# Kernel tuning notes

Hardware: AMD Instinct MI355X
Metric: run time of the kernel (lower is better)

Reference implementation:

```python
import jax, jax.numpy as jnp
import numpy as np

LN_EPS = 1e-5      # torch nn.LayerNorm default
NORM_EPS = 1e-12   # torch F.normalize default


def _layer_norm(x, gamma, beta):
    mu = jnp.mean(x, axis=-1, keepdims=True)
    var = jnp.mean(jnp.square(x - mu), axis=-1, keepdims=True)
    return (x - mu) * jax.lax.rsqrt(var + LN_EPS) * gamma + beta


def setup_inputs() -> dict:
    key = jax.random.key(0)
    ks = jax.random.split(key, 5)
    B, H, W = 4, 480, 712
    N = B * H * W
    x = jax.random.normal(ks[0], (N, 64), dtype=jnp.float32)
    # torch Linear default init ~ U(-1/sqrt(fan_in), 1/sqrt(fan_in)); scaled normals are fine here
    w1 = jax.random.normal(ks[1], (64, 32), dtype=jnp.float32) * (1.0 / np.sqrt(64))
    w2 = jax.random.normal(ks[2], (32, 16), dtype=jnp.float32) * (1.0 / np.sqrt(32))
    w3 = jax.random.normal(ks[3], (16, 3), dtype=jnp.float32) * (1.0 / np.sqrt(16))
    b3 = jax.random.normal(ks[4], (3,), dtype=jnp.float32) * 0.01
    return {
        "x": x,
        "w1": w1, "g1": jnp.ones((32,), jnp.float32), "b1": jnp.zeros((32,), jnp.float32),
        "w2": w2, "g2": jnp.ones((16,), jnp.float32), "b2": jnp.zeros((16,), jnp.float32),
        "w3": w3, "b3": b3,
        "B": B, "H": H, "W": W,
    }


def reference(x, w1, g1, b1, w2, g2, b2, w3, b3, B, H, W):
    # decoder: Linear(64,32,no bias) -> LN(32) -> ReLU -> Linear(32,16,no bias) -> LN(16) -> ReLU -> Linear(16,3)
    h = jax.nn.relu(_layer_norm(x @ w1, g1, b1))
    h = jax.nn.relu(_layer_norm(h @ w2, g2, b2))
    out2d = h @ w3 + b3                      # [B*H*W, 3]
    # reshape_for_layer_norm(..., reverse=True): [B*H*W, C] -> [B, C, H, W]
    out = out2d.reshape(B, H, W, 3).transpose(0, 3, 1, 2)
    # F.normalize(out, dim=1): x / max(||x||_2, eps) along channel dim
    n = jnp.sqrt(jnp.sum(jnp.square(out), axis=1, keepdims=True))
    return out / jnp.maximum(n, NORM_EPS)
```

## Files before the change

### kernel.cpp

```cpp
#include <hip/hip_runtime.h>
#include <stdint.h>

#define LN_EPS 1e-5f

__global__ __launch_bounds__(256, 4) void dec_kernel(
    const float* __restrict__ x,
    const float* __restrict__ w1, const float* __restrict__ g1, const float* __restrict__ b1,
    const float* __restrict__ w2, const float* __restrict__ g2, const float* __restrict__ b2,
    const float* __restrict__ w3, const float* __restrict__ b3,
    float* __restrict__ out, int N, int HW)
{
  const int row = blockIdx.x * 256 + threadIdx.x;
  if (row >= N) return;

  const float4* __restrict__ xp = (const float4*)(x + (size_t)row * 64);

  float4 xv[16];
#pragma unroll
  for (int c = 0; c < 16; ++c) xv[c] = xp[c];

  float acc[32];
#pragma unroll
  for (int j = 0; j < 32; ++j) acc[j] = 0.f;

#pragma unroll
  for (int c = 0; c < 16; ++c) {
#pragma unroll
    for (int kk = 0; kk < 4; ++kk) {
      float xk = (kk == 0) ? xv[c].x : (kk == 1) ? xv[c].y : (kk == 2) ? xv[c].z : xv[c].w;
      const float* wrow = w1 + (c * 4 + kk) * 32;
#pragma unroll
      for (int j = 0; j < 32; ++j) acc[j] = fmaf(xk, wrow[j], acc[j]);
    }
  }

  {
    float p0 = 0.f, p1 = 0.f, p2 = 0.f, p3 = 0.f;
#pragma unroll
    for (int j = 0; j < 32; j += 4) { p0 += acc[j]; p1 += acc[j+1]; p2 += acc[j+2]; p3 += acc[j+3]; }
    float mu = ((p0 + p1) + (p2 + p3)) * 0.03125f;
    float q0 = 0.f, q1 = 0.f, q2 = 0.f, q3 = 0.f;
#pragma unroll
    for (int j = 0; j < 32; j += 4) {
      float d0 = acc[j] - mu, d1 = acc[j+1] - mu, d2 = acc[j+2] - mu, d3 = acc[j+3] - mu;
      acc[j] = d0; acc[j+1] = d1; acc[j+2] = d2; acc[j+3] = d3;
      q0 = fmaf(d0, d0, q0); q1 = fmaf(d1, d1, q1); q2 = fmaf(d2, d2, q2); q3 = fmaf(d3, d3, q3);
    }
    float var = ((q0 + q1) + (q2 + q3)) * 0.03125f;
    float rs  = rsqrtf(var + LN_EPS);
#pragma unroll
    for (int j = 0; j < 32; ++j) {
      float t = acc[j] * rs;
      t = fmaf(t, g1[j], b1[j]);
      acc[j] = fmaxf(t, 0.f);
    }
  }

  float a2[16];
#pragma unroll
  for (int j = 0; j < 16; ++j) a2[j] = 0.f;
#pragma unroll
  for (int k = 0; k < 32; ++k) {
    float hk = acc[k];
    const float* wrow = w2 + k * 16;
#pragma unroll
    for (int j = 0; j < 16; ++j) a2[j] = fmaf(hk, wrow[j], a2[j]);
  }
  {
    float p0 = 0.f, p1 = 0.f, p2 = 0.f, p3 = 0.f;
#pragma unroll
    for (int j = 0; j < 16; j += 4) { p0 += a2[j]; p1 += a2[j+1]; p2 += a2[j+2]; p3 += a2[j+3]; }
    float mu = ((p0 + p1) + (p2 + p3)) * 0.0625f;
    float q0 = 0.f, q1 = 0.f, q2 = 0.f, q3 = 0.f;
#pragma unroll
    for (int j = 0; j < 16; j += 4) {
      float d0 = a2[j] - mu, d1 = a2[j+1] - mu, d2 = a2[j+2] - mu, d3 = a2[j+3] - mu;
      a2[j] = d0; a2[j+1] = d1; a2[j+2] = d2; a2[j+3] = d3;
      q0 = fmaf(d0, d0, q0); q1 = fmaf(d1, d1, q1); q2 = fmaf(d2, d2, q2); q3 = fmaf(d3, d3, q3);
    }
    float var = ((q0 + q1) + (q2 + q3)) * 0.0625f;
    float rs  = rsqrtf(var + LN_EPS);
#pragma unroll
    for (int j = 0; j < 16; ++j) {
      float t = a2[j] * rs;
      t = fmaf(t, g2[j], b2[j]);
      a2[j] = fmaxf(t, 0.f);
    }
  }

  float o0 = b3[0], o1 = b3[1], o2 = b3[2];
#pragma unroll
  for (int k = 0; k < 16; ++k) {
    float hk = a2[k];
    o0 = fmaf(hk, w3[k * 3 + 0], o0);
    o1 = fmaf(hk, w3[k * 3 + 1], o1);
    o2 = fmaf(hk, w3[k * 3 + 2], o2);
  }
  float nsq = fmaf(o0, o0, fmaf(o1, o1, o2 * o2));
  float inv = rsqrtf(fmaxf(nsq, 1e-24f));
  o0 *= inv; o1 *= inv; o2 *= inv;

  int b = (int)((unsigned)row / (unsigned)HW);
  int p = row - b * HW;
  size_t obase = (size_t)b * 3 * HW + p;
  out[obase]          = o0;
  out[obase + HW]     = o1;
  out[obase + 2 * HW] = o2;
}

extern "C" void kernel_launch(void* const* d_in, const int* in_sizes, int n_in,
                              void* d_out, int out_size, void* d_ws, size_t ws_size,
                              hipStream_t stream) {
  const float* x  = (const float*)d_in[0];
  const float* w1 = (const float*)d_in[1];
  const float* g1 = (const float*)d_in[2];
  const float* b1 = (const float*)d_in[3];
  const float* w2 = (const float*)d_in[4];
  const float* g2 = (const float*)d_in[5];
  const float* b2 = (const float*)d_in[6];
  const float* w3 = (const float*)d_in[7];
  const float* b3 = (const float*)d_in[8];
  float* out = (float*)d_out;

  const int N  = in_sizes[0] / 64;
  const int HW = N / 4;
  const int nblocks = (N + 255) / 256;
  dec_kernel<<<nblocks, 256, 0, stream>>>(x, w1, g1, b1, w2, g2, b2, w3, b3, out, N, HW);
}
```

Before: 575.3 us.

## Use persistent grid-stride loop with software-pipelined half-row input prefetch

Launches a fixed grid of up to 1024 blocks that loop over rows in grid-stride order. Each row's 64 floats are loaded in two halves, and the first half of the next row is prefetched while the second half of the current row is being multiplied. sched_barrier calls stop the compiler from reordering loads across these points. The aim is to hide global-load latency with register double-buffering; the cost is higher register pressure, with launch bounds relaxed to 3 blocks per SM and fewer waves in flight.

```diff
diff --git a/kernel.cpp b/kernel.cpp
--- a/kernel.cpp
+++ b/kernel.cpp
@@ -3,109 +3,140 @@
 
 #define LN_EPS 1e-5f
 
-__global__ __launch_bounds__(256, 4) void dec_kernel(
+__global__ __launch_bounds__(256, 3) void dec_kernel(
     const float* __restrict__ x,
     const float* __restrict__ w1, const float* __restrict__ g1, const float* __restrict__ b1,
     const float* __restrict__ w2, const float* __restrict__ g2, const float* __restrict__ b2,
     const float* __restrict__ w3, const float* __restrict__ b3,
     float* __restrict__ out, int N, int HW)
 {
-  const int row = blockIdx.x * 256 + threadIdx.x;
+  const int stride = gridDim.x * 256;
+  int row = blockIdx.x * 256 + threadIdx.x;
   if (row >= N) return;
 
-  const float4* __restrict__ xp = (const float4*)(x + (size_t)row * 64);
+  float4 bufA[8], bufB[8];
+  {
+    const float4* __restrict__ xp = (const float4*)(x + (size_t)row * 64);
+#pragma unroll
+    for (int c = 0; c < 8; ++c) bufA[c] = xp[c];
+  }
 
-  float4 xv[16];
+  while (true) {
+    const float4* __restrict__ xc = (const float4*)(x + (size_t)row * 64);
 #pragma unroll
-  for (int c = 0; c < 16; ++c) xv[c] = xp[c];
+    for (int c = 0; c < 8; ++c) bufB[c] = xc[c + 8];
+    __builtin_amdgcn_sched_barrier(0);
 
-  float acc[32];
+    float acc[32];
 #pragma unroll
-  for (int j = 0; j < 32; ++j) acc[j] = 0.f;
+    for (int j = 0; j < 32; ++j) acc[j] = 0.f;
+#pragma unroll
+    for (int c = 0; c < 8; ++c) {
+#pragma unroll
+      for (int kk = 0; kk < 4; ++kk) {
+        float xk = (kk == 0) ? bufA[c].x : (kk == 1) ? bufA[c].y : (kk == 2) ? bufA[c].z : bufA[c].w;
+        const float* wrow = w1 + (c * 4 + kk) * 32;
+#pragma unroll
+        for (int j = 0; j < 32; ++j) acc[j] = fmaf(xk, wrow[j], acc[j]);
+      }
+    }
+
+    const int nrow = row + stride;
+    {
+      const int prow = (nrow < N) ? nrow : row;
+      const float4* __restrict__ xn = (const float4*)(x + (size_t)prow * 64);
+#pragma unroll
+      for (int c = 0; c < 8; ++c) bufA[c] = xn[c];
+    }
+    __builtin_amdgcn_sched_barrier(0);
 
 #pragma unroll
-  for (int c = 0; c < 16; ++c) {
+    for (int c = 0; c < 8; ++c) {
 #pragma unroll
-    for (int kk = 0; kk < 4; ++kk) {
-      float xk = (kk == 0) ? xv[c].x : (kk == 1) ? xv[c].y : (kk == 2) ? xv[c].z : xv[c].w;
-      const float* wrow = w1 + (c * 4 + kk) * 32;
+      for (int kk = 0; kk < 4; ++kk) {
+        float xk = (kk == 0) ? bufB[c].x : (kk == 1) ? bufB[c].y : (kk == 2) ? bufB[c].z : bufB[c].w;
+        const float* wrow = w1 + (32 + c * 4 + kk) * 32;
 #pragma unroll
-      for (int j = 0; j < 32; ++j) acc[j] = fmaf(xk, wrow[j], acc[j]);
+        for (int j = 0; j < 32; ++j) acc[j] = fmaf(xk, wrow[j], acc[j]);
+      }
     }
+
+    {
+      float p0 = 0.f, p1 = 0.f, p2 = 0.f, p3 = 0.f;
+#pragma unroll
+      for (int j = 0; j < 32; j += 4) { p0 += acc[j]; p1 += acc[j+1]; p2 += acc[j+2]; p3 += acc[j+3]; }
+      float mu = ((p0 + p1) + (p2 + p3)) * 0.03125f;
+      float q0 = 0.f, q1 = 0.f, q2 = 0.f, q3 = 0.f;
+#pragma unroll
+      for (int j = 0; j < 32; j += 4) {
+        float d0 = acc[j] - mu, d1 = acc[j+1] - mu, d2 = acc[j+2] - mu, d3 = acc[j+3] - mu;
+        acc[j] = d0; acc[j+1] = d1; acc[j+2] = d2; acc[j+3] = d3;
+        q0 = fmaf(d0, d0, q0); q1 = fmaf(d1, d1, q1); q2 = fmaf(d2, d2, q2); q3 = fmaf(d3, d3, q3);
+      }
+      float var = ((q0 + q1) + (q2 + q3)) * 0.03125f;
+      float rs  = rsqrtf(var + LN_EPS);
+#pragma unroll
+      for (int j = 0; j < 32; ++j) {
+        float t = acc[j] * rs;
+        t = fmaf(t, g1[j], b1[j]);
+        acc[j] = fmaxf(t, 0.f);
+      }
+    }
+
+    float a2[16];
+#pragma unroll
+    for (int j = 0; j < 16; ++j) a2[j] = 0.f;
+#pragma unroll
+    for (int k = 0; k < 32; ++k) {
+      float hk = acc[k];
+      const float* wrow = w2 + k * 16;
+#pragma unroll
+      for (int j = 0; j < 16; ++j) a2[j] = fmaf(hk, wrow[j], a2[j]);
+    }
+    {
+      float p0 = 0.f, p1 = 0.f, p2 = 0.f, p3 = 0.f;
+#pragma unroll
+      for (int j = 0; j < 16; j += 4) { p0 += a2[j]; p1 += a2[j+1]; p2 += a2[j+2]; p3 += a2[j+3]; }
+      float mu = ((p0 + p1) + (p2 + p3)) * 0.0625f;
+      float q0 = 0.f, q1 = 0.f, q2 = 0.f, q3 = 0.f;
+#pragma unroll
+      for (int j = 0; j < 16; j += 4) {
+        float d0 = a2[j] - mu, d1 = a2[j+1] - mu, d2 = a2[j+2] - mu, d3 = a2[j+3] - mu;
+        a2[j] = d0; a2[j+1] = d1; a2[j+2] = d2; a2[j+3] = d3;
+        q0 = fmaf(d0, d0, q0); q1 = fmaf(d1, d1, q1); q2 = fmaf(d2, d2, q2); q3 = fmaf(d3, d3, q3);
+      }
+      float var = ((q0 + q1) + (q2 + q3)) * 0.0625f;
+      float rs  = rsqrtf(var + LN_EPS);
+#pragma unroll
+      for (int j = 0; j < 16; ++j) {
+        float t = a2[j] * rs;
+        t = fmaf(t, g2[j], b2[j]);
+        a2[j] = fmaxf(t, 0.f);
+      }
+    }
+
+    float o0 = b3[0], o1 = b3[1], o2 = b3[2];
+#pragma unroll
+    for (int k = 0; k < 16; ++k) {
+      float hk = a2[k];
+      o0 = fmaf(hk, w3[k * 3 + 0], o0);
+      o1 = fmaf(hk, w3[k * 3 + 1], o1);
+      o2 = fmaf(hk, w3[k * 3 + 2], o2);
+    }
+    float nsq = fmaf(o0, o0, fmaf(o1, o1, o2 * o2));
+    float inv = rsqrtf(fmaxf(nsq, 1e-24f));
+    o0 *= inv; o1 *= inv; o2 *= inv;
+
+    int b = (int)((unsigned)row / (unsigned)HW);
+    int p = row - b * HW;
+    size_t obase = (size_t)b * 3 * HW + p;
+    out[obase]          = o0;
+    out[obase + HW]     = o1;
+    out[obase + 2 * HW] = o2;
+
+    if (nrow >= N) break;
+    row = nrow;
   }
-
-  {
-    float p0 = 0.f, p1 = 0.f, p2 = 0.f, p3 = 0.f;
-#pragma unroll
-    for (int j = 0; j < 32; j += 4) { p0 += acc[j]; p1 += acc[j+1]; p2 += acc[j+2]; p3 += acc[j+3]; }
-    float mu = ((p0 + p1) + (p2 + p3)) * 0.03125f;
-    float q0 = 0.f, q1 = 0.f, q2 = 0.f, q3 = 0.f;
-#pragma unroll
-    for (int j = 0; j < 32; j += 4) {
-      float d0 = acc[j] - mu, d1 = acc[j+1] - mu, d2 = acc[j+2] - mu, d3 = acc[j+3] - mu;
-      acc[j] = d0; acc[j+1] = d1; acc[j+2] = d2; acc[j+3] = d3;
-      q0 = fmaf(d0, d0, q0); q1 = fmaf(d1, d1, q1); q2 = fmaf(d2, d2, q2); q3 = fmaf(d3, d3, q3);
-    }
-    float var = ((q0 + q1) + (q2 + q3)) * 0.03125f;
-    float rs  = rsqrtf(var + LN_EPS);
-#pragma unroll
-    for (int j = 0; j < 32; ++j) {
-      float t = acc[j] * rs;
-      t = fmaf(t, g1[j], b1[j]);
-      acc[j] = fmaxf(t, 0.f);
-    }
-  }
-
-  float a2[16];
-#pragma unroll
-  for (int j = 0; j < 16; ++j) a2[j] = 0.f;
-#pragma unroll
-  for (int k = 0; k < 32; ++k) {
-    float hk = acc[k];
-    const float* wrow = w2 + k * 16;
-#pragma unroll
-    for (int j = 0; j < 16; ++j) a2[j] = fmaf(hk, wrow[j], a2[j]);
-  }
-  {
-    float p0 = 0.f, p1 = 0.f, p2 = 0.f, p3 = 0.f;
-#pragma unroll
-    for (int j = 0; j < 16; j += 4) { p0 += a2[j]; p1 += a2[j+1]; p2 += a2[j+2]; p3 += a2[j+3]; }
-    float mu = ((p0 + p1) + (p2 + p3)) * 0.0625f;
-    float q0 = 0.f, q1 = 0.f, q2 = 0.f, q3 = 0.f;
-#pragma unroll
-    for (int j = 0; j < 16; j += 4) {
-      float d0 = a2[j] - mu, d1 = a2[j+1] - mu, d2 = a2[j+2] - mu, d3 = a2[j+3] - mu;
-      a2[j] = d0; a2[j+1] = d1; a2[j+2] = d2; a2[j+3] = d3;
-      q0 = fmaf(d0, d0, q0); q1 = fmaf(d1, d1, q1); q2 = fmaf(d2, d2, q2); q3 = fmaf(d3, d3, q3);
-    }
-    float var = ((q0 + q1) + (q2 + q3)) * 0.0625f;
-    float rs  = rsqrtf(var + LN_EPS);
-#pragma unroll
-    for (int j = 0; j < 16; ++j) {
-      float t = a2[j] * rs;
-      t = fmaf(t, g2[j], b2[j]);
-      a2[j] = fmaxf(t, 0.f);
-    }
-  }
-
-  float o0 = b3[0], o1 = b3[1], o2 = b3[2];
-#pragma unroll
-  for (int k = 0; k < 16; ++k) {
-    float hk = a2[k];
-    o0 = fmaf(hk, w3[k * 3 + 0], o0);
-    o1 = fmaf(hk, w3[k * 3 + 1], o1);
-    o2 = fmaf(hk, w3[k * 3 + 2], o2);
-  }
-  float nsq = fmaf(o0, o0, fmaf(o1, o1, o2 * o2));
-  float inv = rsqrtf(fmaxf(nsq, 1e-24f));
-  o0 *= inv; o1 *= inv; o2 *= inv;
-
-  int b = (int)((unsigned)row / (unsigned)HW);
-  int p = row - b * HW;
-  size_t obase = (size_t)b * 3 * HW + p;
-  out[obase]          = o0;
-  out[obase + HW]     = o1;
-  out[obase + 2 * HW] = o2;
 }
 
 extern "C" void kernel_launch(void* const* d_in, const int* in_sizes, int n_in,
@@ -124,6 +155,8 @@
 
   const int N  = in_sizes[0] / 64;
   const int HW = N / 4;
-  const int nblocks = (N + 255) / 256;
+  int nblocks = 1024;
+  const int maxb = (N + 255) / 256;
+  if (nblocks > maxb) nblocks = maxb;
   dec_kernel<<<nblocks, 256, 0, stream>>>(x, w1, g1, b1, w2, g2, b2, w3, b3, out, N, HW);
 }
```

Result: slower. 1.194 ms (+107.6%).
